# Kernel optimization log

Hardware: AMD Instinct MI355X
Metric: run time of the kernel (lower is better)

## Reference

```python
import jax, jax.numpy as jnp
import numpy as np

B, IN_DIM, EXP_DIM, E = 16384, 256, 128, 8  # batch, input_dim, expert_dim, expert_num


def setup_inputs() -> dict:
    key = jax.random.key(0)
    ks = jax.random.split(key, 12)
    s_in = 1.0 / np.sqrt(IN_DIM)
    return {
        "x_a": jax.random.normal(ks[0], (B, IN_DIM), jnp.float32),
        "x_b": jax.random.normal(ks[1], (B, IN_DIM), jnp.float32),
        "x_share": jax.random.normal(ks[2], (B, IN_DIM), jnp.float32),
        # expert banks: [E, IN_DIM, EXP_DIM] weights, [E, EXP_DIM] bias
        "Wa": jax.random.uniform(ks[3], (E, IN_DIM, EXP_DIM), jnp.float32, -s_in, s_in),
        "ba": jax.random.uniform(ks[4], (E, EXP_DIM), jnp.float32, -s_in, s_in),
        "Wb": jax.random.uniform(ks[5], (E, IN_DIM, EXP_DIM), jnp.float32, -s_in, s_in),
        "bb": jax.random.uniform(ks[6], (E, EXP_DIM), jnp.float32, -s_in, s_in),
        "Ws": jax.random.uniform(ks[7], (E, IN_DIM, EXP_DIM), jnp.float32, -s_in, s_in),
        "bs": jax.random.uniform(ks[8], (E, EXP_DIM), jnp.float32, -s_in, s_in),
        # gate projections (bias=False): num single-output linears == one [num, IN_DIM] matrix
        "Ga": jax.random.uniform(ks[9], (2 * E, IN_DIM), jnp.float32, -s_in, s_in),
        "Gb": jax.random.uniform(ks[10], (2 * E, IN_DIM), jnp.float32, -s_in, s_in),
        "Gs": jax.random.uniform(ks[11], (3 * E, IN_DIM), jnp.float32, -s_in, s_in),
    }


def _experts(x, W, b):
    # batched dense stack: [B,IN] x [E,IN,D] -> [B,E,D]
    return jnp.einsum("bi,eid->bed", x, W) + b[None, :, :]


def _gate(x, G, experts):
    # logits [B, num]; softmax over experts; weighted sum over expert axis
    w = jax.nn.softmax(x @ G.T, axis=1)
    return jnp.einsum("be,bed->bd", w, experts)


def reference(x_a, x_b, x_share, Wa, ba, Wb, bb, Ws, bs, Ga, Gb, Gs):
    ea = _experts(x_a, Wa, ba)          # [B,E,D]
    eb = _experts(x_b, Wb, bb)          # [B,E,D]
    es = _experts(x_share, Ws, bs)      # [B,E,D]
    out_a = _gate(x_a, Ga, jnp.concatenate([ea, es], axis=1))
    out_b = _gate(x_b, Gb, jnp.concatenate([eb, es], axis=1))
    out_s = _gate(x_share, Gs, jnp.concatenate([ea, eb, es], axis=1))
    return (out_a, out_b, out_s)
```

## Files before the change

### kernel.cpp

```cpp
#include <hip/hip_runtime.h>
#include <stdint.h>

#define BATCH 16384
#define INDIM 256
#define DDIM  128
#define NEXP  8
#define ROWS  64
#define THREADS 512
#define NSEQ  48
#define SLABE 16384

typedef __bf16 bfv8  __attribute__((ext_vector_type(8)));
typedef float  f32x4 __attribute__((ext_vector_type(4)));

typedef __attribute__((address_space(1))) const void gas_void;
typedef __attribute__((address_space(3))) void las_void;

__global__ void prep_kernel(const float* __restrict__ Wa, const float* __restrict__ Wb,
                            const float* __restrict__ Ws, const float* __restrict__ Ga,
                            const float* __restrict__ Gb, const float* __restrict__ Gs,
                            __bf16* __restrict__ wp, __bf16* __restrict__ gp) {
    __shared__ float ws[32 * 132];
    const int b = blockIdx.x, tid = threadIdx.x;
    if (b < 192) {
        const int st = b >> 6, e = (b >> 3) & 7, kt = b & 7;
        const float* W = (st == 0) ? Wa : (st == 1) ? Wb : Ws;
        const float* src = W + (size_t)(e * 256 + kt * 32) * 128;
#pragma unroll
        for (int k = 0; k < 4; k++) {
            int idx4 = tid + k * 256;
            f32x4 v = *(const f32x4*)(src + (size_t)idx4 * 4);
            int row = idx4 >> 5;
            int col = (idx4 & 31) << 2;
            ws[row * 132 + col + 0] = v[0];
            ws[row * 132 + col + 1] = v[1];
            ws[row * 132 + col + 2] = v[2];
            ws[row * 132 + col + 3] = v[3];
        }
        __syncthreads();
        __bf16* o = wp + ((size_t)b << 12);
#pragma unroll
        for (int h2 = 0; h2 < 2; h2++) {
            int base = tid * 2 + h2;
            int nt = base >> 6, lane = base & 63;
            int d  = nt * 16 + (lane & 15);
            int i0 = (lane >> 4) * 8;
            bfv8 ov;
#pragma unroll
            for (int j = 0; j < 8; j++) ov[j] = (__bf16)ws[(i0 + j) * 132 + d];
            *(bfv8*)(o + (size_t)base * 8) = ov;
        }
    } else {
        int t2 = (b - 192) * 256 + tid;
        int lane = t2 & 63, nt = (t2 >> 6) & 3, kt = t2 >> 8;
        int g  = nt * 16 + (lane & 15);
        int k0 = kt * 32 + (lane >> 4) * 8;
        __bf16* o = gp + (size_t)t2 * 8;
#pragma unroll
        for (int j = 0; j < 8; j++) {
            int k = k0 + j;
            float v = 0.f;
            if (g < 16)      v = Ga[g * 256 + k];
            else if (g < 32) v = Gb[(g - 16) * 256 + k];
            else if (g < 56) v = Gs[(g - 32) * 256 + k];
            o[j] = (__bf16)v;
        }
    }
}

__device__ __forceinline__ void load_afr(const float* __restrict__ x, int rb,
                                         int l16, int quad, bfv8 afr[2][8]) {
#pragma unroll
    for (int mt = 0; mt < 2; mt++) {
        const float* xr = x + (size_t)(rb + mt * 16 + l16) * INDIM;
#pragma unroll
        for (int kt = 0; kt < 8; kt++) {
            const f32x4* p = (const f32x4*)(xr + kt * 32 + quad * 8);
            f32x4 lo = __builtin_nontemporal_load(p);
            f32x4 hi = __builtin_nontemporal_load(p + 1);
            bfv8 a;
            a[0] = (__bf16)lo[0]; a[1] = (__bf16)lo[1]; a[2] = (__bf16)lo[2]; a[3] = (__bf16)lo[3];
            a[4] = (__bf16)hi[0]; a[5] = (__bf16)hi[1]; a[6] = (__bf16)hi[2]; a[7] = (__bf16)hi[3];
            afr[mt][kt] = a;
        }
    }
}

__device__ __forceinline__ void stage_slab(const __bf16* __restrict__ wp,
                                           __bf16* ring, int hslab, int slot,
                                           int wv, int lane) {
    const __bf16* src = wp + ((size_t)hslab << 14) + (wv << 11) + (lane << 3);
    __bf16* dst = ring + (slot << 14) + (wv << 11);
#pragma unroll
    for (int i = 0; i < 4; i++)
        __builtin_amdgcn_global_load_lds((gas_void*)(src + (i << 9)),
                                         (las_void*)(dst + (i << 9)), 16, 0, 0);
}

__device__ __forceinline__ int slab_of(int s, int rot) {
    int st = s >> 4, r = s & 15;
    int eb = (((r >> 1) + rot) & 7);
    return (st << 4) | (eb << 1) | (s & 1);
}

__launch_bounds__(THREADS, 2)
__global__ void ple_kernel(const float* __restrict__ xa, const float* __restrict__ xb,
                           const float* __restrict__ xs,
                           const float* __restrict__ ba, const float* __restrict__ bb,
                           const float* __restrict__ bs,
                           const __bf16* __restrict__ wp, const __bf16* __restrict__ gp,
                           float* __restrict__ out) {
    __shared__ __bf16 ring[2 * SLABE];
    __shared__ float lgt[ROWS * 64];
    __shared__ float wT[64 * ROWS];

    const int tid  = threadIdx.x;
    const int wv   = tid >> 6;
    const int lane = tid & 63;
    const int rg   = wv >> 2;
    const int cg   = wv & 3;
    const int quad = lane >> 4;
    const int l16  = lane & 15;
    const int r0   = blockIdx.x * ROWS;
    const int rb   = r0 + rg * 32;
    const int rot  = (blockIdx.x >> 3) & 7;

    stage_slab(wp, ring, slab_of(0, rot), 0, wv, lane);

    bfv8 afr[2][8];

    {
        const float* x = (cg == 0) ? xa : (cg == 1) ? xb : xs;
        load_afr(x, rb, l16, quad, afr);
        f32x4 acc1[2];
#pragma unroll
        for (int mt = 0; mt < 2; mt++) { f32x4 z = {0.f, 0.f, 0.f, 0.f}; acc1[mt] = z; }
#pragma unroll
        for (int kt = 0; kt < 8; kt++) {
            bfv8 gfr = *(const bfv8*)(gp + ((size_t)(kt * 4 + cg) * 64 + lane) * 8);
#pragma unroll
            for (int mt = 0; mt < 2; mt++)
                acc1[mt] = __builtin_amdgcn_mfma_f32_16x16x32_bf16(afr[mt][kt], gfr, acc1[mt], 0, 0, 0);
        }
#pragma unroll
        for (int mt = 0; mt < 2; mt++)
#pragma unroll
            for (int r = 0; r < 4; r++)
                lgt[(rg * 32 + mt * 16 + quad * 4 + r) * 64 + cg * 16 + l16] = acc1[mt][r];
    }
    __syncthreads();

    if (tid < ROWS) {
        const float* L = lgt + tid * 64;
#pragma unroll
        for (int gi = 0; gi < 3; gi++) {
            const int base = (gi == 0) ? 0 : (gi == 1 ? 16 : 32);
            const int cnt  = (gi == 2) ? 24 : 16;
            float m = -1e30f;
            for (int k = 0; k < cnt; k++) m = fmaxf(m, L[base + k]);
            float s = 0.f;
            for (int k = 0; k < cnt; k++) s += __expf(L[base + k] - m);
            float inv = 1.f / s;
            for (int k = 0; k < cnt; k++) wT[(base + k) * ROWS + tid] = __expf(L[base + k] - m) * inv;
        }
    }
    __syncthreads();

    float o[3][2][2][4];
#pragma unroll
    for (int oi = 0; oi < 3; oi++)
#pragma unroll
        for (int mt = 0; mt < 2; mt++)
#pragma unroll
            for (int ntl = 0; ntl < 2; ntl++)
#pragma unroll
                for (int r = 0; r < 4; r++) o[oi][mt][ntl][r] = 0.f;

#define FOLD(oi, gbase)                                                                 \
    {                                                                                   \
        _Pragma("unroll")                                                               \
        for (int mt = 0; mt < 2; mt++) {                                                \
            f32x4 gw4 = *(const f32x4*)(wT + (gbase + eb) * ROWS + rg * 32 + mt * 16 + quad * 4); \
            _Pragma("unroll")                                                           \
            for (int ntl = 0; ntl < 2; ntl++)                                           \
                _Pragma("unroll")                                                       \
                for (int r = 0; r < 4; r++)                                             \
                    o[oi][mt][ntl][r] += gw4[r] * acc[mt][ntl][r];                      \
        }                                                                               \
    }

#pragma unroll
    for (int st = 0; st < 3; st++) {
        const float* x    = (st == 0) ? xa : (st == 1) ? xb : xs;
        const float* bias = (st == 0) ? ba : (st == 1) ? bb : bs;
        load_afr(x, rb, l16, quad, afr);

#pragma unroll 1
        for (int eb0 = 0; eb0 < NEXP; eb0++) {
            const int eb = (eb0 + rot) & 7;
            float b0 = bias[eb * 128 + cg * 32 + l16];
            float b1 = bias[eb * 128 + cg * 32 + 16 + l16];

            f32x4 acc[2][2];
#pragma unroll
            for (int mt = 0; mt < 2; mt++)
#pragma unroll
                for (int ntl = 0; ntl < 2; ntl++) { f32x4 z = {0.f, 0.f, 0.f, 0.f}; acc[mt][ntl] = z; }

#pragma unroll
            for (int half = 0; half < 2; half++) {
                const int s = st * 16 + eb0 * 2 + half;
                __syncthreads();
                if (s + 1 < NSEQ)
                    stage_slab(wp, ring, slab_of(s + 1, rot), (s + 1) & 1, wv, lane);

                const __bf16* buf = ring + (half << 14);
#pragma unroll
                for (int kt4 = 0; kt4 < 4; kt4++) {
                    const int kt = half * 4 + kt4;
                    const __bf16* slab = buf + (kt4 << 12) + (cg << 10);
                    bfv8 bv0 = *(const bfv8*)(slab + ((size_t)lane << 3));
                    bfv8 bv1 = *(const bfv8*)(slab + 512 + ((size_t)lane << 3));
                    acc[0][0] = __builtin_amdgcn_mfma_f32_16x16x32_bf16(afr[0][kt], bv0, acc[0][0], 0, 0, 0);
                    acc[1][0] = __builtin_amdgcn_mfma_f32_16x16x32_bf16(afr[1][kt], bv0, acc[1][0], 0, 0, 0);
                    acc[0][1] = __builtin_amdgcn_mfma_f32_16x16x32_bf16(afr[0][kt], bv1, acc[0][1], 0, 0, 0);
                    acc[1][1] = __builtin_amdgcn_mfma_f32_16x16x32_bf16(afr[1][kt], bv1, acc[1][1], 0, 0, 0);
                }
            }

#pragma unroll
            for (int mt = 0; mt < 2; mt++)
#pragma unroll
                for (int r = 0; r < 4; r++) { acc[mt][0][r] += b0; acc[mt][1][r] += b1; }

            if (st == 0)      { FOLD(0, 0);  FOLD(2, 32); }
            else if (st == 1) { FOLD(1, 16); FOLD(2, 40); }
            else              { FOLD(0, 8);  FOLD(1, 24); FOLD(2, 48); }
        }
    }
#undef FOLD

#pragma unroll
    for (int oi = 0; oi < 3; oi++) {
        float* ob = out + (size_t)oi * BATCH * DDIM;
#pragma unroll
        for (int mt = 0; mt < 2; mt++)
#pragma unroll
            for (int r = 0; r < 4; r++) {
                int row = rb + mt * 16 + quad * 4 + r;
#pragma unroll
                for (int ntl = 0; ntl < 2; ntl++)
                    __builtin_nontemporal_store(o[oi][mt][ntl][r],
                        &ob[(size_t)row * DDIM + cg * 32 + ntl * 16 + l16]);
            }
    }
}

extern "C" void kernel_launch(void* const* d_in, const int* in_sizes, int n_in,
                              void* d_out, int out_size, void* d_ws, size_t ws_size,
                              hipStream_t stream) {
    const float* xa = (const float*)d_in[0];
    const float* xb = (const float*)d_in[1];
    const float* xs = (const float*)d_in[2];
    const float* Wa = (const float*)d_in[3];
    const float* ba = (const float*)d_in[4];
    const float* Wb = (const float*)d_in[5];
    const float* bb = (const float*)d_in[6];
    const float* Ws = (const float*)d_in[7];
    const float* bs = (const float*)d_in[8];
    const float* Ga = (const float*)d_in[9];
    const float* Gb = (const float*)d_in[10];
    const float* Gs = (const float*)d_in[11];

    __bf16* wp = (__bf16*)d_ws;
    __bf16* gp = wp + 3 * 8 * 8 * 8 * 64 * 8;

    prep_kernel<<<200, 256, 0, stream>>>(Wa, Wb, Ws, Ga, Gb, Gs, wp, gp);
    ple_kernel<<<BATCH / ROWS, THREADS, 0, stream>>>(xa, xb, xs, ba, bb, bs, wp, gp, (float*)d_out);
}
```

Baseline: 180.7 us.

## Give each wave a private weight ring staged with per-wave waitcnt, no block barriers

Halves the block to 32 rows and 4 waves and raises the occupancy hint to 4 blocks per CU. Each wave now streams its own column slice of the expert weights into a private double-buffered LDS region and syncs with s_waitcnt vmcnt instead of __syncthreads, which removes block-wide barriers from the inner loop. It also raises wave priority around the MFMA sections and overlays the logits buffer on the ring. In exchange each wave reloads weights for fewer rows, so weight traffic per output row doubles, and correctness depends on the hand-tuned vmcnt counts matching what the compiler emits.

```diff
diff --git a/kernel.cpp b/kernel.cpp
--- a/kernel.cpp
+++ b/kernel.cpp
@@ -5,10 +5,9 @@
 #define INDIM 256
 #define DDIM  128
 #define NEXP  8
-#define ROWS  64
-#define THREADS 512
-#define NSEQ  48
-#define SLABE 16384
+#define ROWS  32
+#define THREADS 256
+#define NSTEP 96
 
 typedef __bf16 bfv8  __attribute__((ext_vector_type(8)));
 typedef float  f32x4 __attribute__((ext_vector_type(4)));
@@ -86,46 +85,41 @@
     }
 }
 
-__device__ __forceinline__ void stage_slab(const __bf16* __restrict__ wp,
-                                           __bf16* ring, int hslab, int slot,
-                                           int wv, int lane) {
-    const __bf16* src = wp + ((size_t)hslab << 14) + (wv << 11) + (lane << 3);
-    __bf16* dst = ring + (slot << 14) + (wv << 11);
-#pragma unroll
-    for (int i = 0; i < 4; i++)
-        __builtin_amdgcn_global_load_lds((gas_void*)(src + (i << 9)),
-                                         (las_void*)(dst + (i << 9)), 16, 0, 0);
-}
-
-__device__ __forceinline__ int slab_of(int s, int rot) {
-    int st = s >> 4, r = s & 15;
-    int eb = (((r >> 1) + rot) & 7);
-    return (st << 4) | (eb << 1) | (s & 1);
-}
-
-__launch_bounds__(THREADS, 2)
+__device__ __forceinline__ void stage_step(const __bf16* __restrict__ wp,
+                                           __bf16* pbuf, int st, int eb, int q,
+                                           int slot, int cg, int lane) {
+    const __bf16* src = wp + (((size_t)(st * 64 + eb * 8 + q * 2)) << 12)
+                           + (cg << 10) + (lane << 3);
+    __bf16* d = pbuf + (slot << 11);
+#pragma unroll
+    for (int j = 0; j < 2; j++)
+#pragma unroll
+        for (int sub = 0; sub < 2; sub++)
+            __builtin_amdgcn_global_load_lds(
+                (gas_void*)(src + (j << 12) + (sub << 9)),
+                (las_void*)(d + (j << 10) + (sub << 9)), 16, 0, 0);
+}
+
+__launch_bounds__(THREADS, 4)
 __global__ void ple_kernel(const float* __restrict__ xa, const float* __restrict__ xb,
                            const float* __restrict__ xs,
                            const float* __restrict__ ba, const float* __restrict__ bb,
                            const float* __restrict__ bs,
                            const __bf16* __restrict__ wp, const __bf16* __restrict__ gp,
                            float* __restrict__ out) {
-    __shared__ __bf16 ring[2 * SLABE];
-    __shared__ float lgt[ROWS * 64];
-    __shared__ float wT[64 * ROWS];
+    __shared__ __align__(16) unsigned char smem[40960];
+    __bf16* ring = (__bf16*)smem;
+    float*  wT   = (float*)(smem + 32768);
+    float*  lgt  = (float*)smem;
 
     const int tid  = threadIdx.x;
     const int wv   = tid >> 6;
     const int lane = tid & 63;
-    const int rg   = wv >> 2;
-    const int cg   = wv & 3;
+    const int cg   = wv;
     const int quad = lane >> 4;
     const int l16  = lane & 15;
-    const int r0   = blockIdx.x * ROWS;
-    const int rb   = r0 + rg * 32;
+    const int rb   = blockIdx.x * ROWS;
     const int rot  = (blockIdx.x >> 3) & 7;
-
-    stage_slab(wp, ring, slab_of(0, rot), 0, wv, lane);
 
     bfv8 afr[2][8];
 
@@ -146,7 +140,7 @@
         for (int mt = 0; mt < 2; mt++)
 #pragma unroll
             for (int r = 0; r < 4; r++)
-                lgt[(rg * 32 + mt * 16 + quad * 4 + r) * 64 + cg * 16 + l16] = acc1[mt][r];
+                lgt[(mt * 16 + quad * 4 + r) * 64 + cg * 16 + l16] = acc1[mt][r];
     }
     __syncthreads();
 
@@ -166,6 +160,8 @@
     }
     __syncthreads();
 
+    __bf16* pbuf = ring + (wv << 12);
+
     float o[3][2][2][4];
 #pragma unroll
     for (int oi = 0; oi < 3; oi++)
@@ -180,7 +176,7 @@
     {                                                                                   \
         _Pragma("unroll")                                                               \
         for (int mt = 0; mt < 2; mt++) {                                                \
-            f32x4 gw4 = *(const f32x4*)(wT + (gbase + eb) * ROWS + rg * 32 + mt * 16 + quad * 4); \
+            f32x4 gw4 = *(const f32x4*)(wT + (gbase + eb) * ROWS + mt * 16 + quad * 4); \
             _Pragma("unroll")                                                           \
             for (int ntl = 0; ntl < 2; ntl++)                                           \
                 _Pragma("unroll")                                                       \
@@ -189,6 +185,8 @@
         }                                                                               \
     }
 
+    stage_step(wp, pbuf, 0, rot & 7, 0, 0, cg, lane);
+
 #pragma unroll
     for (int st = 0; st < 3; st++) {
         const float* x    = (st == 0) ? xa : (st == 1) ? xb : xs;
@@ -208,24 +206,32 @@
                 for (int ntl = 0; ntl < 2; ntl++) { f32x4 z = {0.f, 0.f, 0.f, 0.f}; acc[mt][ntl] = z; }
 
 #pragma unroll
-            for (int half = 0; half < 2; half++) {
-                const int s = st * 16 + eb0 * 2 + half;
-                __syncthreads();
-                if (s + 1 < NSEQ)
-                    stage_slab(wp, ring, slab_of(s + 1, rot), (s + 1) & 1, wv, lane);
-
-                const __bf16* buf = ring + (half << 14);
-#pragma unroll
-                for (int kt4 = 0; kt4 < 4; kt4++) {
-                    const int kt = half * 4 + kt4;
-                    const __bf16* slab = buf + (kt4 << 12) + (cg << 10);
-                    bfv8 bv0 = *(const bfv8*)(slab + ((size_t)lane << 3));
-                    bfv8 bv1 = *(const bfv8*)(slab + 512 + ((size_t)lane << 3));
+            for (int q = 0; q < 4; q++) {
+                const int s = st * 32 + eb0 * 4 + q;
+                if (s + 1 < NSTEP) {
+                    const int s1 = s + 1, st1 = s1 >> 5, r1 = s1 & 31;
+                    stage_step(wp, pbuf, st1, ((r1 >> 2) + rot) & 7, r1 & 3,
+                               s1 & 1, cg, lane);
+                    if (q == 0) asm volatile("s_waitcnt vmcnt(6)" ::: "memory");
+                    else        asm volatile("s_waitcnt vmcnt(4)" ::: "memory");
+                } else {
+                    asm volatile("s_waitcnt vmcnt(0)" ::: "memory");
+                }
+                __builtin_amdgcn_sched_barrier(0);
+
+                const __bf16* pb = pbuf + ((s & 1) << 11);
+                __builtin_amdgcn_s_setprio(1);
+#pragma unroll
+                for (int j = 0; j < 2; j++) {
+                    const int kt = q * 2 + j;
+                    bfv8 bv0 = *(const bfv8*)(pb + (j << 10) + ((size_t)lane << 3));
+                    bfv8 bv1 = *(const bfv8*)(pb + (j << 10) + 512 + ((size_t)lane << 3));
                     acc[0][0] = __builtin_amdgcn_mfma_f32_16x16x32_bf16(afr[0][kt], bv0, acc[0][0], 0, 0, 0);
                     acc[1][0] = __builtin_amdgcn_mfma_f32_16x16x32_bf16(afr[1][kt], bv0, acc[1][0], 0, 0, 0);
                     acc[0][1] = __builtin_amdgcn_mfma_f32_16x16x32_bf16(afr[0][kt], bv1, acc[0][1], 0, 0, 0);
                     acc[1][1] = __builtin_amdgcn_mfma_f32_16x16x32_bf16(afr[1][kt], bv1, acc[1][1], 0, 0, 0);
                 }
+                __builtin_amdgcn_s_setprio(0);
             }
 
 #pragma unroll
```

After: 217.7 us. 1.21x slower.

## Split output columns across two blocks per row tile to double grid size

Applied to the files above, without the earlier changes.

Each 64-row tile is now handled by two blocks, each computing half of the 128 output columns. Each wave covers a 16-row by 32-column sub-tile instead of 32 by 32, and the LDS weight ring is halved. This doubles the number of blocks and lowers LDS and register use per block, which should raise occupancy and parallelism. In exchange, both blocks recompute the gate logits and softmax and each reloads the full x rows, so activation reads and gating work are duplicated.

```diff
diff --git a/kernel.cpp b/kernel.cpp
--- a/kernel.cpp
+++ b/kernel.cpp
@@ -8,7 +8,7 @@
 #define ROWS  64
 #define THREADS 512
 #define NSEQ  48
-#define SLABE 16384
+#define HSLAB 8192
 
 typedef __bf16 bfv8  __attribute__((ext_vector_type(8)));
 typedef float  f32x4 __attribute__((ext_vector_type(4)));
@@ -86,20 +86,36 @@
     }
 }
 
-__device__ __forceinline__ void stage_slab(const __bf16* __restrict__ wp,
-                                           __bf16* ring, int hslab, int slot,
-                                           int wv, int lane) {
-    const __bf16* src = wp + ((size_t)hslab << 14) + (wv << 11) + (lane << 3);
-    __bf16* dst = ring + (slot << 14) + (wv << 11);
-#pragma unroll
-    for (int i = 0; i < 4; i++)
+__device__ __forceinline__ void load_afr16(const float* __restrict__ x, int rbase,
+                                           int l16, int quad, bfv8 afr[8]) {
+    const float* xr = x + (size_t)(rbase + l16) * INDIM;
+#pragma unroll
+    for (int kt = 0; kt < 8; kt++) {
+        const f32x4* p = (const f32x4*)(xr + kt * 32 + quad * 8);
+        f32x4 lo = __builtin_nontemporal_load(p);
+        f32x4 hi = __builtin_nontemporal_load(p + 1);
+        bfv8 a;
+        a[0] = (__bf16)lo[0]; a[1] = (__bf16)lo[1]; a[2] = (__bf16)lo[2]; a[3] = (__bf16)lo[3];
+        a[4] = (__bf16)hi[0]; a[5] = (__bf16)hi[1]; a[6] = (__bf16)hi[2]; a[7] = (__bf16)hi[3];
+        afr[kt] = a;
+    }
+}
+
+__device__ __forceinline__ void stage_h(const __bf16* __restrict__ wp,
+                                        __bf16* ring, int hs, int slot,
+                                        int co, int wv, int lane) {
+    const __bf16* src = wp + ((size_t)(hs * 4 + (wv >> 1)) << 12)
+                           + (co << 11) + ((wv & 1) << 10) + (lane << 3);
+    __bf16* dst = ring + (slot << 13) + ((size_t)wv << 10);
+#pragma unroll
+    for (int i = 0; i < 2; i++)
         __builtin_amdgcn_global_load_lds((gas_void*)(src + (i << 9)),
                                          (las_void*)(dst + (i << 9)), 16, 0, 0);
 }
 
-__device__ __forceinline__ int slab_of(int s, int rot) {
-    int st = s >> 4, r = s & 15;
-    int eb = (((r >> 1) + rot) & 7);
+__device__ __forceinline__ int hs_of(int s, int rot) {
+    int st = s >> 4;
+    int eb = (((s >> 1) & 7) + rot) & 7;
     return (st << 4) | (eb << 1) | (s & 1);
 }
 
@@ -110,26 +126,27 @@
                            const float* __restrict__ bs,
                            const __bf16* __restrict__ wp, const __bf16* __restrict__ gp,
                            float* __restrict__ out) {
-    __shared__ __bf16 ring[2 * SLABE];
+    __shared__ __bf16 ring[2 * HSLAB];
     __shared__ float lgt[ROWS * 64];
     __shared__ float wT[64 * ROWS];
 
     const int tid  = threadIdx.x;
     const int wv   = tid >> 6;
     const int lane = tid & 63;
-    const int rg   = wv >> 2;
-    const int cg   = wv & 3;
     const int quad = lane >> 4;
     const int l16  = lane & 15;
-    const int r0   = blockIdx.x * ROWS;
-    const int rb   = r0 + rg * 32;
-    const int rot  = (blockIdx.x >> 3) & 7;
-
-    stage_slab(wp, ring, slab_of(0, rot), 0, wv, lane);
-
-    bfv8 afr[2][8];
+    const int bid  = blockIdx.x;
+    const int r0   = (bid >> 1) * ROWS;
+    const int co   = bid & 1;
+    const int rot  = (bid >> 3) & 7;
+
+    stage_h(wp, ring, hs_of(0, rot), 0, co, wv, lane);
 
     {
+        const int rg = wv >> 2;
+        const int cg = wv & 3;
+        const int rb = r0 + rg * 32;
+        bfv8 afr[2][8];
         const float* x = (cg == 0) ? xa : (cg == 1) ? xb : xs;
         load_afr(x, rb, l16, quad, afr);
         f32x4 acc1[2];
@@ -166,72 +183,66 @@
     }
     __syncthreads();
 
-    float o[3][2][2][4];
+    const int rg2   = wv >> 1;
+    const int cgl   = wv & 1;
+    const int rbase = r0 + rg2 * 16;
+
+    bfv8 afr2[8];
+    float o[3][2][4];
 #pragma unroll
     for (int oi = 0; oi < 3; oi++)
 #pragma unroll
-        for (int mt = 0; mt < 2; mt++)
-#pragma unroll
-            for (int ntl = 0; ntl < 2; ntl++)
-#pragma unroll
-                for (int r = 0; r < 4; r++) o[oi][mt][ntl][r] = 0.f;
-
-#define FOLD(oi, gbase)                                                                 \
-    {                                                                                   \
-        _Pragma("unroll")                                                               \
-        for (int mt = 0; mt < 2; mt++) {                                                \
-            f32x4 gw4 = *(const f32x4*)(wT + (gbase + eb) * ROWS + rg * 32 + mt * 16 + quad * 4); \
-            _Pragma("unroll")                                                           \
-            for (int ntl = 0; ntl < 2; ntl++)                                           \
-                _Pragma("unroll")                                                       \
-                for (int r = 0; r < 4; r++)                                             \
-                    o[oi][mt][ntl][r] += gw4[r] * acc[mt][ntl][r];                      \
-        }                                                                               \
+        for (int ntl = 0; ntl < 2; ntl++)
+#pragma unroll
+            for (int r = 0; r < 4; r++) o[oi][ntl][r] = 0.f;
+
+#define FOLD(oi, gbase)                                                              \
+    {                                                                                \
+        f32x4 gw4 = *(const f32x4*)(wT + (gbase + eb) * ROWS + rg2 * 16 + quad * 4); \
+        _Pragma("unroll")                                                            \
+        for (int ntl = 0; ntl < 2; ntl++)                                            \
+            _Pragma("unroll")                                                        \
+            for (int r = 0; r < 4; r++)                                              \
+                o[oi][ntl][r] += gw4[r] * acc[ntl][r];                               \
     }
 
 #pragma unroll
     for (int st = 0; st < 3; st++) {
         const float* x    = (st == 0) ? xa : (st == 1) ? xb : xs;
         const float* bias = (st == 0) ? ba : (st == 1) ? bb : bs;
-        load_afr(x, rb, l16, quad, afr);
+        load_afr16(x, rbase, l16, quad, afr2);
 
 #pragma unroll 1
         for (int eb0 = 0; eb0 < NEXP; eb0++) {
             const int eb = (eb0 + rot) & 7;
-            float b0 = bias[eb * 128 + cg * 32 + l16];
-            float b1 = bias[eb * 128 + cg * 32 + 16 + l16];
-
-            f32x4 acc[2][2];
-#pragma unroll
-            for (int mt = 0; mt < 2; mt++)
-#pragma unroll
-                for (int ntl = 0; ntl < 2; ntl++) { f32x4 z = {0.f, 0.f, 0.f, 0.f}; acc[mt][ntl] = z; }
+            float b0 = bias[eb * 128 + co * 64 + cgl * 32 + l16];
+            float b1 = bias[eb * 128 + co * 64 + cgl * 32 + 16 + l16];
+
+            f32x4 acc[2];
+#pragma unroll
+            for (int ntl = 0; ntl < 2; ntl++) { f32x4 z = {0.f, 0.f, 0.f, 0.f}; acc[ntl] = z; }
 
 #pragma unroll
             for (int half = 0; half < 2; half++) {
                 const int s = st * 16 + eb0 * 2 + half;
                 __syncthreads();
                 if (s + 1 < NSEQ)
-                    stage_slab(wp, ring, slab_of(s + 1, rot), (s + 1) & 1, wv, lane);
-
-                const __bf16* buf = ring + (half << 14);
+                    stage_h(wp, ring, hs_of(s + 1, rot), (s + 1) & 1, co, wv, lane);
+
+                const __bf16* buf = ring + ((s & 1) << 13);
 #pragma unroll
                 for (int kt4 = 0; kt4 < 4; kt4++) {
                     const int kt = half * 4 + kt4;
-                    const __bf16* slab = buf + (kt4 << 12) + (cg << 10);
-                    bfv8 bv0 = *(const bfv8*)(slab + ((size_t)lane << 3));
-                    bfv8 bv1 = *(const bfv8*)(slab + 512 + ((size_t)lane << 3));
-                    acc[0][0] = __builtin_amdgcn_mfma_f32_16x16x32_bf16(afr[0][kt], bv0, acc[0][0], 0, 0, 0);
-                    acc[1][0] = __builtin_amdgcn_mfma_f32_16x16x32_bf16(afr[1][kt], bv0, acc[1][0], 0, 0, 0);
-                    acc[0][1] = __builtin_amdgcn_mfma_f32_16x16x32_bf16(afr[0][kt], bv1, acc[0][1], 0, 0, 0);
-                    acc[1][1] = __builtin_amdgcn_mfma_f32_16x16x32_bf16(afr[1][kt], bv1, acc[1][1], 0, 0, 0);
+                    const __bf16* reg = buf + (kt4 << 11) + (cgl << 10);
+                    bfv8 bv0 = *(const bfv8*)(reg + ((size_t)lane << 3));
+                    bfv8 bv1 = *(const bfv8*)(reg + 512 + ((size_t)lane << 3));
+                    acc[0] = __builtin_amdgcn_mfma_f32_16x16x32_bf16(afr2[kt], bv0, acc[0], 0, 0, 0);
+                    acc[1] = __builtin_amdgcn_mfma_f32_16x16x32_bf16(afr2[kt], bv1, acc[1], 0, 0, 0);
                 }
             }
 
 #pragma unroll
-            for (int mt = 0; mt < 2; mt++)
-#pragma unroll
-                for (int r = 0; r < 4; r++) { acc[mt][0][r] += b0; acc[mt][1][r] += b1; }
+            for (int r = 0; r < 4; r++) { acc[0][r] += b0; acc[1][r] += b1; }
 
             if (st == 0)      { FOLD(0, 0);  FOLD(2, 32); }
             else if (st == 1) { FOLD(1, 16); FOLD(2, 40); }
@@ -244,15 +255,13 @@
     for (int oi = 0; oi < 3; oi++) {
         float* ob = out + (size_t)oi * BATCH * DDIM;
 #pragma unroll
-        for (int mt = 0; mt < 2; mt++)
-#pragma unroll
-            for (int r = 0; r < 4; r++) {
-                int row = rb + mt * 16 + quad * 4 + r;
-#pragma unroll
-                for (int ntl = 0; ntl < 2; ntl++)
-                    __builtin_nontemporal_store(o[oi][mt][ntl][r],
-                        &ob[(size_t)row * DDIM + cg * 32 + ntl * 16 + l16]);
-            }
+        for (int r = 0; r < 4; r++) {
+            int row = rbase + quad * 4 + r;
+#pragma unroll
+            for (int ntl = 0; ntl < 2; ntl++)
+                __builtin_nontemporal_store(o[oi][ntl][r],
+                    &ob[(size_t)row * DDIM + co * 64 + cgl * 32 + ntl * 16 + l16]);
+        }
     }
 }
 
@@ -276,5 +285,5 @@
     __bf16* gp = wp + 3 * 8 * 8 * 8 * 64 * 8;
 
     prep_kernel<<<200, 256, 0, stream>>>(Wa, Wb, Ws, Ga, Gb, Gs, wp, gp);
-    ple_kernel<<<BATCH / ROWS, THREADS, 0, stream>>>(xa, xb, xs, ba, bb, bs, wp, gp, (float*)d_out);
-}
+    ple_kernel<<<2 * (BATCH / ROWS), THREADS, 0, stream>>>(xa, xb, xs, ba, bb, bs, wp, gp, (float*)d_out);
+}
```

Measured after the change: 203.7 us. 1.13x slower.
